# Optimization experiments

Hardware: AMD Instinct MI355X
Metric: run time of the kernel (lower is better)

Reference implementation:

```python
import jax, jax.numpy as jnp
import numpy as np

_DIMS = [("fu1",2,2),("fu2",2,2),("ku1",4,4),("ku2",4,4),("hu1",6,6),("hu2",6,6),("md1",11,16),("md2",16,16),("md3",16,6),("hd1",6,4),("hd2",4,4),("kd1",4,2),("kd2",2,2),("ha1",8,4),("ha2",4,1),("ka1",6,4),("ka2",4,1),("fa1",4,4),("fa2",4,1)]


def setup_inputs() -> dict:
    key = jax.random.key(0)
    B = 2_000_000
    inp = {"x": jax.random.normal(key, (B, 11), dtype=jnp.float32)}
    for i, (name, din, dout) in enumerate(_DIMS):
        kw = jax.random.fold_in(key, i + 1)
        scale = float(np.sqrt(6.0 / (din + dout)))  # xavier_uniform gain=1
        inp[name + "_w"] = jax.random.uniform(kw, (din, dout), jnp.float32, -scale, scale)
        inp[name + "_b"] = jnp.zeros((dout,), jnp.float32)  # nn.Linear default bias ~ small; zeros for determinism
    return inp


def _lin(x, w, b):
    # weights stored as (in, out) == torch W.T
    return x @ w + b


def reference(x, fu1_w, fu1_b, fu2_w, fu2_b, ku1_w, ku1_b, ku2_w, ku2_b, hu1_w, hu1_b, hu2_w, hu2_b, md1_w, md1_b, md2_w, md2_b, md3_w, md3_b, hd1_w, hd1_b, hd2_w, hd2_b, kd1_w, kd1_b, kd2_w, kd2_b, ha1_w, ha1_b, ha2_w, ha2_b, ka1_w, ka1_b, ka2_w, ka2_b, fa1_w, fa1_b, fa2_w, fa2_b):
    r = jax.nn.relu
    h = x[:, 2:3]; k = x[:, 3:4]; f = x[:, 4:5]
    hd = x[:, 8:9]; kd = x[:, 9:10]; fd = x[:, 10:11]
    m_obs = x[:, jnp.array([0, 1, 5, 6, 7])]  # [B,5]
    f_up = r(_lin(r(_lin(jnp.concatenate([f, fd], 1), fu1_w, fu1_b)), fu2_w, fu2_b))            # [B,2]
    k_up = r(_lin(r(_lin(jnp.concatenate([k, kd, f_up], 1), ku1_w, ku1_b)), ku2_w, ku2_b))      # [B,4]
    h_up = r(_lin(r(_lin(jnp.concatenate([h, hd, k_up], 1), hu1_w, hu1_b)), hu2_w, hu2_b))      # [B,6]
    m_in = jnp.concatenate([m_obs, h_up], 1)                                                    # [B,11]
    m_down = r(_lin(r(_lin(r(_lin(m_in, md1_w, md1_b)), md2_w, md2_b)), md3_w, md3_b))          # [B,6]
    h_down = r(_lin(r(_lin(m_down, hd1_w, hd1_b)), hd2_w, hd2_b))                               # [B,4]
    k_down = r(_lin(r(_lin(h_down, kd1_w, kd1_b)), kd2_w, kd2_b))                               # [B,2]
    h_act = _lin(r(_lin(jnp.concatenate([h, hd, m_down], 1), ha1_w, ha1_b)), ha2_w, ha2_b)      # [B,1]
    k_act = _lin(r(_lin(jnp.concatenate([k, kd, h_down], 1), ka1_w, ka1_b)), ka2_w, ka2_b)      # [B,1]
    f_act = _lin(r(_lin(jnp.concatenate([f, fd, k_down], 1), fa1_w, fa1_b)), fa2_w, fa2_b)      # [B,1]
    return jnp.concatenate([h_act, f_act, k_act], 1)                                            # [B,3]
```

## Files before the change

### kernel.cpp

```cpp
#include <hip/hip_runtime.h>

#define BLOCK 256

typedef float v2f __attribute__((ext_vector_type(2)));
typedef unsigned long long u64;

struct WPtrs {
    const float* w[19];
    const float* b[19];
};

enum LId {FU1,FU2,KU1,KU2,HU1,HU2,MD1,MD2,MD3,HD1,HD2,KD1,KD2,HA1,HA2,KA1,KA2,FA1,FA2};

__device__ __forceinline__ void fmaL(v2f& acc, const v2f s, const u64 w) {
    asm("v_pk_fma_f32 %0, %1, %2, %0 op_sel:[0,0,0] op_sel_hi:[0,1,1]"
        : "+v"(acc) : "v"(s), "s"(w));
}
__device__ __forceinline__ void fmaH(v2f& acc, const v2f s, const u64 w) {
    asm("v_pk_fma_f32 %0, %1, %2, %0 op_sel:[1,0,0] op_sel_hi:[1,1,1]"
        : "+v"(acc) : "v"(s), "s"(w));
}
__device__ __forceinline__ v2f pkmax0(const v2f a) {
    const v2f z = {0.0f, 0.0f};
    return __builtin_elementwise_max(a, z);
}
__device__ __forceinline__ v2f bias2(const float* b, int jp) {
    return *reinterpret_cast<const v2f*>(b + 2*jp);
}

__global__ __launch_bounds__(BLOCK) void pnet_kernel(
    const float* __restrict__ x, float* __restrict__ out, int B, WPtrs P) {
    const long long row = (long long)blockIdx.x * BLOCK + threadIdx.x;
    if (row >= B) return;

    const float* pr = x + row * 11;
    const v2f xp01 = *reinterpret_cast<const v2f*>(pr + 0);
    const v2f xp23 = *reinterpret_cast<const v2f*>(pr + 2);
    const v2f xp45 = *reinterpret_cast<const v2f*>(pr + 4);
    const v2f xp67 = *reinterpret_cast<const v2f*>(pr + 6);
    const v2f xp89 = *reinterpret_cast<const v2f*>(pr + 8);
    const v2f xp9A = *reinterpret_cast<const v2f*>(pr + 9);

    v2f fu1p;
    {
        const u64* wp = reinterpret_cast<const u64*>(P.w[FU1]);
        v2f a = bias2(P.b[FU1], 0);
        fmaL(a, xp45, wp[0]);
        fmaH(a, xp9A, wp[1]);
        fu1p = pkmax0(a);
    }
    v2f fup;
    {
        const u64* wp = reinterpret_cast<const u64*>(P.w[FU2]);
        v2f a = bias2(P.b[FU2], 0);
        fmaL(a, fu1p, wp[0]);
        fmaH(a, fu1p, wp[1]);
        fup = pkmax0(a);
    }

    v2f ku1p[2];
    {
        const u64* wp = reinterpret_cast<const u64*>(P.w[KU1]);
#pragma unroll
        for (int jp = 0; jp < 2; ++jp) {
            v2f a = bias2(P.b[KU1], jp);
            fmaH(a, xp23, wp[0*2+jp]);
            fmaH(a, xp89, wp[1*2+jp]);
            fmaL(a, fup,  wp[2*2+jp]);
            fmaH(a, fup,  wp[3*2+jp]);
            ku1p[jp] = pkmax0(a);
        }
    }
    v2f kup[2];
    {
        const u64* wp = reinterpret_cast<const u64*>(P.w[KU2]);
#pragma unroll
        for (int jp = 0; jp < 2; ++jp) {
            v2f a = bias2(P.b[KU2], jp);
            fmaL(a, ku1p[0], wp[0*2+jp]);
            fmaH(a, ku1p[0], wp[1*2+jp]);
            fmaL(a, ku1p[1], wp[2*2+jp]);
            fmaH(a, ku1p[1], wp[3*2+jp]);
            kup[jp] = pkmax0(a);
        }
    }

    v2f hu1p[3];
    {
        const u64* wp = reinterpret_cast<const u64*>(P.w[HU1]);
#pragma unroll
        for (int jp = 0; jp < 3; ++jp) {
            v2f a = bias2(P.b[HU1], jp);
            fmaL(a, xp23,   wp[0*3+jp]);
            fmaL(a, xp89,   wp[1*3+jp]);
            fmaL(a, kup[0], wp[2*3+jp]);
            fmaH(a, kup[0], wp[3*3+jp]);
            fmaL(a, kup[1], wp[4*3+jp]);
            fmaH(a, kup[1], wp[5*3+jp]);
            hu1p[jp] = pkmax0(a);
        }
    }
    v2f hup[3];
    {
        const u64* wp = reinterpret_cast<const u64*>(P.w[HU2]);
#pragma unroll
        for (int jp = 0; jp < 3; ++jp) {
            v2f a = bias2(P.b[HU2], jp);
            fmaL(a, hu1p[0], wp[0*3+jp]);
            fmaH(a, hu1p[0], wp[1*3+jp]);
            fmaL(a, hu1p[1], wp[2*3+jp]);
            fmaH(a, hu1p[1], wp[3*3+jp]);
            fmaL(a, hu1p[2], wp[4*3+jp]);
            fmaH(a, hu1p[2], wp[5*3+jp]);
            hup[jp] = pkmax0(a);
        }
    }

    v2f m1[8];
    {
        const u64* wp = reinterpret_cast<const u64*>(P.w[MD1]);
#pragma unroll
        for (int jp = 0; jp < 8; ++jp) {
            v2f a = bias2(P.b[MD1], jp);
            fmaL(a, xp01,   wp[0*8+jp]);
            fmaH(a, xp01,   wp[1*8+jp]);
            fmaH(a, xp45,   wp[2*8+jp]);
            fmaL(a, xp67,   wp[3*8+jp]);
            fmaH(a, xp67,   wp[4*8+jp]);
            fmaL(a, hup[0], wp[5*8+jp]);
            fmaH(a, hup[0], wp[6*8+jp]);
            fmaL(a, hup[1], wp[7*8+jp]);
            fmaH(a, hup[1], wp[8*8+jp]);
            fmaL(a, hup[2], wp[9*8+jp]);
            fmaH(a, hup[2], wp[10*8+jp]);
            m1[jp] = pkmax0(a);
        }
    }
    v2f m2[8];
    {
        const u64* wp = reinterpret_cast<const u64*>(P.w[MD2]);
#pragma unroll
        for (int jp = 0; jp < 8; ++jp) {
            v2f a = bias2(P.b[MD2], jp);
#pragma unroll
            for (int p = 0; p < 8; ++p) {
                fmaL(a, m1[p], wp[(2*p)  *8+jp]);
                fmaH(a, m1[p], wp[(2*p+1)*8+jp]);
            }
            m2[jp] = pkmax0(a);
        }
    }
    v2f m3[3];
    {
        const u64* wp = reinterpret_cast<const u64*>(P.w[MD3]);
#pragma unroll
        for (int jp = 0; jp < 3; ++jp) {
            v2f a = bias2(P.b[MD3], jp);
#pragma unroll
            for (int p = 0; p < 8; ++p) {
                fmaL(a, m2[p], wp[(2*p)  *3+jp]);
                fmaH(a, m2[p], wp[(2*p+1)*3+jp]);
            }
            m3[jp] = pkmax0(a);
        }
    }

    v2f d1[2];
    {
        const u64* wp = reinterpret_cast<const u64*>(P.w[HD1]);
#pragma unroll
        for (int jp = 0; jp < 2; ++jp) {
            v2f a = bias2(P.b[HD1], jp);
            fmaL(a, m3[0], wp[0*2+jp]);
            fmaH(a, m3[0], wp[1*2+jp]);
            fmaL(a, m3[1], wp[2*2+jp]);
            fmaH(a, m3[1], wp[3*2+jp]);
            fmaL(a, m3[2], wp[4*2+jp]);
            fmaH(a, m3[2], wp[5*2+jp]);
            d1[jp] = pkmax0(a);
        }
    }
    v2f d2[2];
    {
        const u64* wp = reinterpret_cast<const u64*>(P.w[HD2]);
#pragma unroll
        for (int jp = 0; jp < 2; ++jp) {
            v2f a = bias2(P.b[HD2], jp);
            fmaL(a, d1[0], wp[0*2+jp]);
            fmaH(a, d1[0], wp[1*2+jp]);
            fmaL(a, d1[1], wp[2*2+jp]);
            fmaH(a, d1[1], wp[3*2+jp]);
            d2[jp] = pkmax0(a);
        }
    }

    v2f e1;
    {
        const u64* wp = reinterpret_cast<const u64*>(P.w[KD1]);
        v2f a = bias2(P.b[KD1], 0);
        fmaL(a, d2[0], wp[0]);
        fmaH(a, d2[0], wp[1]);
        fmaL(a, d2[1], wp[2]);
        fmaH(a, d2[1], wp[3]);
        e1 = pkmax0(a);
    }
    v2f e2;
    {
        const u64* wp = reinterpret_cast<const u64*>(P.w[KD2]);
        v2f a = bias2(P.b[KD2], 0);
        fmaL(a, e1, wp[0]);
        fmaH(a, e1, wp[1]);
        e2 = pkmax0(a);
    }

    v2f g[2];
    {
        const u64* wp = reinterpret_cast<const u64*>(P.w[HA1]);
#pragma unroll
        for (int jp = 0; jp < 2; ++jp) {
            v2f a = bias2(P.b[HA1], jp);
            fmaL(a, xp23,  wp[0*2+jp]);
            fmaL(a, xp89,  wp[1*2+jp]);
            fmaL(a, m3[0], wp[2*2+jp]);
            fmaH(a, m3[0], wp[3*2+jp]);
            fmaL(a, m3[1], wp[4*2+jp]);
            fmaH(a, m3[1], wp[5*2+jp]);
            fmaL(a, m3[2], wp[6*2+jp]);
            fmaH(a, m3[2], wp[7*2+jp]);
            g[jp] = pkmax0(a);
        }
    }
    const float* wha = P.w[HA2];
    float h_act = P.b[HA2][0];
    h_act = __builtin_fmaf(g[0].x, wha[0], h_act);
    h_act = __builtin_fmaf(g[0].y, wha[1], h_act);
    h_act = __builtin_fmaf(g[1].x, wha[2], h_act);
    h_act = __builtin_fmaf(g[1].y, wha[3], h_act);

    v2f q[2];
    {
        const u64* wp = reinterpret_cast<const u64*>(P.w[KA1]);
#pragma unroll
        for (int jp = 0; jp < 2; ++jp) {
            v2f a = bias2(P.b[KA1], jp);
            fmaH(a, xp23,  wp[0*2+jp]);
            fmaH(a, xp89,  wp[1*2+jp]);
            fmaL(a, d2[0], wp[2*2+jp]);
            fmaH(a, d2[0], wp[3*2+jp]);
            fmaL(a, d2[1], wp[4*2+jp]);
            fmaH(a, d2[1], wp[5*2+jp]);
            q[jp] = pkmax0(a);
        }
    }
    const float* wka = P.w[KA2];
    float k_act = P.b[KA2][0];
    k_act = __builtin_fmaf(q[0].x, wka[0], k_act);
    k_act = __builtin_fmaf(q[0].y, wka[1], k_act);
    k_act = __builtin_fmaf(q[1].x, wka[2], k_act);
    k_act = __builtin_fmaf(q[1].y, wka[3], k_act);

    v2f r[2];
    {
        const u64* wp = reinterpret_cast<const u64*>(P.w[FA1]);
#pragma unroll
        for (int jp = 0; jp < 2; ++jp) {
            v2f a = bias2(P.b[FA1], jp);
            fmaL(a, xp45, wp[0*2+jp]);
            fmaH(a, xp9A, wp[1*2+jp]);
            fmaL(a, e2,   wp[2*2+jp]);
            fmaH(a, e2,   wp[3*2+jp]);
            r[jp] = pkmax0(a);
        }
    }
    const float* wfa = P.w[FA2];
    float f_act = P.b[FA2][0];
    f_act = __builtin_fmaf(r[0].x, wfa[0], f_act);
    f_act = __builtin_fmaf(r[0].y, wfa[1], f_act);
    f_act = __builtin_fmaf(r[1].x, wfa[2], f_act);
    f_act = __builtin_fmaf(r[1].y, wfa[3], f_act);

    float* po = out + row * 3;
    po[0] = h_act;
    po[1] = f_act;
    po[2] = k_act;
}

extern "C" void kernel_launch(void* const* d_in, const int* in_sizes, int n_in,
                              void* d_out, int out_size, void* d_ws, size_t ws_size,
                              hipStream_t stream) {
    const float* x = (const float*)d_in[0];
    float* out = (float*)d_out;
    const int B = in_sizes[0] / 11;

    WPtrs P;
    for (int i = 0; i < 19; ++i) {
        P.w[i] = (const float*)d_in[1 + 2*i];
        P.b[i] = (const float*)d_in[2 + 2*i];
    }

    const int blocks = (int)(((long long)B + BLOCK - 1) / BLOCK);
    pnet_kernel<<<blocks, BLOCK, 0, stream>>>(x, out, B, P);
}
```

Before: 229.6 us.

## Pack all weights and biases into one contiguous stream via prep kernel

Adds a small prep kernel that repacks the 19 layers' weights and biases into a single contiguous workspace buffer, laid out in the order the main kernel reads them (bias pair followed by the weight pairs for each output pair). The main kernel then takes one pointer and uses compile-time offsets. This is meant to turn many scattered scalar loads from 38 separate pointers into sequential wide scalar loads from a single base, cutting SGPR pressure and load instruction count. In exchange it adds a second kernel launch on every call.

```diff
diff --git a/kernel.cpp b/kernel.cpp
--- a/kernel.cpp
+++ b/kernel.cpp
@@ -10,7 +10,36 @@
     const float* b[19];
 };
 
-enum LId {FU1,FU2,KU1,KU2,HU1,HU2,MD1,MD2,MD3,HD1,HD2,KD1,KD2,HA1,HA2,KA1,KA2,FA1,FA2};
+__constant__ const int kDIN[19]  = {2,2,4,4,6,6,11,16,16,6,4,4,2,8,4,6,4,4,4};
+__constant__ const int kDOUT[19] = {2,2,4,4,6,6,16,16,6,4,4,2,2,4,1,4,1,4,1};
+__constant__ const int kOFF[19]  = {0,3,6,16,26,47,68,164,300,351,365,375,380,383,401,404,418,421,431};
+
+__global__ void prep_kernel(WPtrs P, float* __restrict__ ws) {
+    const int l = blockIdx.x;
+    const int t = threadIdx.x;
+    const int din = kDIN[l], dout = kDOUT[l];
+    const int off = kOFF[l];
+    if (dout == 1) {
+        if (t == 0) {
+            float* d = ws + 2*off;
+            d[0] = P.b[l][0];
+            for (int i = 0; i < 4; ++i) d[1+i] = P.w[l][i];
+            d[5] = 0.0f;
+        }
+        return;
+    }
+    const int pairs  = dout >> 1;
+    const int stride = 1 + din;
+    for (int jp = t; jp < pairs; jp += blockDim.x) {
+        float* d = ws + 2*(off + jp*stride);
+        d[0] = P.b[l][2*jp];
+        d[1] = P.b[l][2*jp + 1];
+        for (int i = 0; i < din; ++i) {
+            d[2 + 2*i] = P.w[l][i*dout + 2*jp];
+            d[3 + 2*i] = P.w[l][i*dout + 2*jp + 1];
+        }
+    }
+}
 
 __device__ __forceinline__ void fmaL(v2f& acc, const v2f s, const u64 w) {
     asm("v_pk_fma_f32 %0, %1, %2, %0 op_sel:[0,0,0] op_sel_hi:[0,1,1]"
@@ -24,14 +53,17 @@
     const v2f z = {0.0f, 0.0f};
     return __builtin_elementwise_max(a, z);
 }
-__device__ __forceinline__ v2f bias2(const float* b, int jp) {
-    return *reinterpret_cast<const v2f*>(b + 2*jp);
+__device__ __forceinline__ v2f bcv(const u64 v) {
+    return __builtin_bit_cast(v2f, v);
 }
 
 __global__ __launch_bounds__(BLOCK) void pnet_kernel(
-    const float* __restrict__ x, float* __restrict__ out, int B, WPtrs P) {
+    const float* __restrict__ x, float* __restrict__ out, int B,
+    const float* __restrict__ wstream) {
     const long long row = (long long)blockIdx.x * BLOCK + threadIdx.x;
     if (row >= B) return;
+
+    const u64* W = reinterpret_cast<const u64*>(wstream);
 
     const float* pr = x + row * 11;
     const v2f xp01 = *reinterpret_cast<const v2f*>(pr + 0);
@@ -43,241 +75,210 @@
 
     v2f fu1p;
     {
-        const u64* wp = reinterpret_cast<const u64*>(P.w[FU1]);
-        v2f a = bias2(P.b[FU1], 0);
-        fmaL(a, xp45, wp[0]);
-        fmaH(a, xp9A, wp[1]);
+        v2f a = bcv(W[0]);
+        fmaL(a, xp45, W[1]);
+        fmaH(a, xp9A, W[2]);
         fu1p = pkmax0(a);
     }
     v2f fup;
     {
-        const u64* wp = reinterpret_cast<const u64*>(P.w[FU2]);
-        v2f a = bias2(P.b[FU2], 0);
-        fmaL(a, fu1p, wp[0]);
-        fmaH(a, fu1p, wp[1]);
+        v2f a = bcv(W[3]);
+        fmaL(a, fu1p, W[4]);
+        fmaH(a, fu1p, W[5]);
         fup = pkmax0(a);
     }
 
     v2f ku1p[2];
-    {
-        const u64* wp = reinterpret_cast<const u64*>(P.w[KU1]);
-#pragma unroll
-        for (int jp = 0; jp < 2; ++jp) {
-            v2f a = bias2(P.b[KU1], jp);
-            fmaH(a, xp23, wp[0*2+jp]);
-            fmaH(a, xp89, wp[1*2+jp]);
-            fmaL(a, fup,  wp[2*2+jp]);
-            fmaH(a, fup,  wp[3*2+jp]);
-            ku1p[jp] = pkmax0(a);
+#pragma unroll
+    for (int jp = 0; jp < 2; ++jp) {
+        const int q = 6 + jp*5;
+        v2f a = bcv(W[q]);
+        fmaH(a, xp23, W[q+1]);
+        fmaH(a, xp89, W[q+2]);
+        fmaL(a, fup,  W[q+3]);
+        fmaH(a, fup,  W[q+4]);
+        ku1p[jp] = pkmax0(a);
+    }
+    v2f kup[2];
+#pragma unroll
+    for (int jp = 0; jp < 2; ++jp) {
+        const int q = 16 + jp*5;
+        v2f a = bcv(W[q]);
+        fmaL(a, ku1p[0], W[q+1]);
+        fmaH(a, ku1p[0], W[q+2]);
+        fmaL(a, ku1p[1], W[q+3]);
+        fmaH(a, ku1p[1], W[q+4]);
+        kup[jp] = pkmax0(a);
+    }
+
+    v2f hu1p[3];
+#pragma unroll
+    for (int jp = 0; jp < 3; ++jp) {
+        const int q = 26 + jp*7;
+        v2f a = bcv(W[q]);
+        fmaL(a, xp23,   W[q+1]);
+        fmaL(a, xp89,   W[q+2]);
+        fmaL(a, kup[0], W[q+3]);
+        fmaH(a, kup[0], W[q+4]);
+        fmaL(a, kup[1], W[q+5]);
+        fmaH(a, kup[1], W[q+6]);
+        hu1p[jp] = pkmax0(a);
+    }
+    v2f hup[3];
+#pragma unroll
+    for (int jp = 0; jp < 3; ++jp) {
+        const int q = 47 + jp*7;
+        v2f a = bcv(W[q]);
+        fmaL(a, hu1p[0], W[q+1]);
+        fmaH(a, hu1p[0], W[q+2]);
+        fmaL(a, hu1p[1], W[q+3]);
+        fmaH(a, hu1p[1], W[q+4]);
+        fmaL(a, hu1p[2], W[q+5]);
+        fmaH(a, hu1p[2], W[q+6]);
+        hup[jp] = pkmax0(a);
+    }
+
+    v2f m1[8];
+#pragma unroll
+    for (int jp = 0; jp < 8; ++jp) {
+        const int q = 68 + jp*12;
+        v2f a = bcv(W[q]);
+        fmaL(a, xp01,   W[q+1]);
+        fmaH(a, xp01,   W[q+2]);
+        fmaH(a, xp45,   W[q+3]);
+        fmaL(a, xp67,   W[q+4]);
+        fmaH(a, xp67,   W[q+5]);
+        fmaL(a, hup[0], W[q+6]);
+        fmaH(a, hup[0], W[q+7]);
+        fmaL(a, hup[1], W[q+8]);
+        fmaH(a, hup[1], W[q+9]);
+        fmaL(a, hup[2], W[q+10]);
+        fmaH(a, hup[2], W[q+11]);
+        m1[jp] = pkmax0(a);
+    }
+    v2f m2[8];
+#pragma unroll
+    for (int jp = 0; jp < 8; ++jp) {
+        const int q = 164 + jp*17;
+        v2f a = bcv(W[q]);
+#pragma unroll
+        for (int p = 0; p < 8; ++p) {
+            fmaL(a, m1[p], W[q + 1 + 2*p]);
+            fmaH(a, m1[p], W[q + 2 + 2*p]);
         }
-    }
-    v2f kup[2];
-    {
-        const u64* wp = reinterpret_cast<const u64*>(P.w[KU2]);
-#pragma unroll
-        for (int jp = 0; jp < 2; ++jp) {
-            v2f a = bias2(P.b[KU2], jp);
-            fmaL(a, ku1p[0], wp[0*2+jp]);
-            fmaH(a, ku1p[0], wp[1*2+jp]);
-            fmaL(a, ku1p[1], wp[2*2+jp]);
-            fmaH(a, ku1p[1], wp[3*2+jp]);
-            kup[jp] = pkmax0(a);
+        m2[jp] = pkmax0(a);
+    }
+    v2f m3[3];
+#pragma unroll
+    for (int jp = 0; jp < 3; ++jp) {
+        const int q = 300 + jp*17;
+        v2f a = bcv(W[q]);
+#pragma unroll
+        for (int p = 0; p < 8; ++p) {
+            fmaL(a, m2[p], W[q + 1 + 2*p]);
+            fmaH(a, m2[p], W[q + 2 + 2*p]);
         }
-    }
-
-    v2f hu1p[3];
-    {
-        const u64* wp = reinterpret_cast<const u64*>(P.w[HU1]);
-#pragma unroll
-        for (int jp = 0; jp < 3; ++jp) {
-            v2f a = bias2(P.b[HU1], jp);
-            fmaL(a, xp23,   wp[0*3+jp]);
-            fmaL(a, xp89,   wp[1*3+jp]);
-            fmaL(a, kup[0], wp[2*3+jp]);
-            fmaH(a, kup[0], wp[3*3+jp]);
-            fmaL(a, kup[1], wp[4*3+jp]);
-            fmaH(a, kup[1], wp[5*3+jp]);
-            hu1p[jp] = pkmax0(a);
-        }
-    }
-    v2f hup[3];
-    {
-        const u64* wp = reinterpret_cast<const u64*>(P.w[HU2]);
-#pragma unroll
-        for (int jp = 0; jp < 3; ++jp) {
-            v2f a = bias2(P.b[HU2], jp);
-            fmaL(a, hu1p[0], wp[0*3+jp]);
-            fmaH(a, hu1p[0], wp[1*3+jp]);
-            fmaL(a, hu1p[1], wp[2*3+jp]);
-            fmaH(a, hu1p[1], wp[3*3+jp]);
-            fmaL(a, hu1p[2], wp[4*3+jp]);
-            fmaH(a, hu1p[2], wp[5*3+jp]);
-            hup[jp] = pkmax0(a);
-        }
-    }
-
-    v2f m1[8];
-    {
-        const u64* wp = reinterpret_cast<const u64*>(P.w[MD1]);
-#pragma unroll
-        for (int jp = 0; jp < 8; ++jp) {
-            v2f a = bias2(P.b[MD1], jp);
-            fmaL(a, xp01,   wp[0*8+jp]);
-            fmaH(a, xp01,   wp[1*8+jp]);
-            fmaH(a, xp45,   wp[2*8+jp]);
-            fmaL(a, xp67,   wp[3*8+jp]);
-            fmaH(a, xp67,   wp[4*8+jp]);
-            fmaL(a, hup[0], wp[5*8+jp]);
-            fmaH(a, hup[0], wp[6*8+jp]);
-            fmaL(a, hup[1], wp[7*8+jp]);
-            fmaH(a, hup[1], wp[8*8+jp]);
-            fmaL(a, hup[2], wp[9*8+jp]);
-            fmaH(a, hup[2], wp[10*8+jp]);
-            m1[jp] = pkmax0(a);
-        }
-    }
-    v2f m2[8];
-    {
-        const u64* wp = reinterpret_cast<const u64*>(P.w[MD2]);
-#pragma unroll
-        for (int jp = 0; jp < 8; ++jp) {
-            v2f a = bias2(P.b[MD2], jp);
-#pragma unroll
-            for (int p = 0; p < 8; ++p) {
-                fmaL(a, m1[p], wp[(2*p)  *8+jp]);
-                fmaH(a, m1[p], wp[(2*p+1)*8+jp]);
-            }
-            m2[jp] = pkmax0(a);
-        }
-    }
-    v2f m3[3];
-    {
-        const u64* wp = reinterpret_cast<const u64*>(P.w[MD3]);
-#pragma unroll
-        for (int jp = 0; jp < 3; ++jp) {
-            v2f a = bias2(P.b[MD3], jp);
-#pragma unroll
-            for (int p = 0; p < 8; ++p) {
-                fmaL(a, m2[p], wp[(2*p)  *3+jp]);
-                fmaH(a, m2[p], wp[(2*p+1)*3+jp]);
-            }
-            m3[jp] = pkmax0(a);
-        }
+        m3[jp] = pkmax0(a);
     }
 
     v2f d1[2];
-    {
-        const u64* wp = reinterpret_cast<const u64*>(P.w[HD1]);
-#pragma unroll
-        for (int jp = 0; jp < 2; ++jp) {
-            v2f a = bias2(P.b[HD1], jp);
-            fmaL(a, m3[0], wp[0*2+jp]);
-            fmaH(a, m3[0], wp[1*2+jp]);
-            fmaL(a, m3[1], wp[2*2+jp]);
-            fmaH(a, m3[1], wp[3*2+jp]);
-            fmaL(a, m3[2], wp[4*2+jp]);
-            fmaH(a, m3[2], wp[5*2+jp]);
-            d1[jp] = pkmax0(a);
-        }
+#pragma unroll
+    for (int jp = 0; jp < 2; ++jp) {
+        const int q = 351 + jp*7;
+        v2f a = bcv(W[q]);
+        fmaL(a, m3[0], W[q+1]);
+        fmaH(a, m3[0], W[q+2]);
+        fmaL(a, m3[1], W[q+3]);
+        fmaH(a, m3[1], W[q+4]);
+        fmaL(a, m3[2], W[q+5]);
+        fmaH(a, m3[2], W[q+6]);
+        d1[jp] = pkmax0(a);
     }
     v2f d2[2];
-    {
-        const u64* wp = reinterpret_cast<const u64*>(P.w[HD2]);
-#pragma unroll
-        for (int jp = 0; jp < 2; ++jp) {
-            v2f a = bias2(P.b[HD2], jp);
-            fmaL(a, d1[0], wp[0*2+jp]);
-            fmaH(a, d1[0], wp[1*2+jp]);
-            fmaL(a, d1[1], wp[2*2+jp]);
-            fmaH(a, d1[1], wp[3*2+jp]);
-            d2[jp] = pkmax0(a);
-        }
+#pragma unroll
+    for (int jp = 0; jp < 2; ++jp) {
+        const int q = 365 + jp*5;
+        v2f a = bcv(W[q]);
+        fmaL(a, d1[0], W[q+1]);
+        fmaH(a, d1[0], W[q+2]);
+        fmaL(a, d1[1], W[q+3]);
+        fmaH(a, d1[1], W[q+4]);
+        d2[jp] = pkmax0(a);
     }
 
     v2f e1;
     {
-        const u64* wp = reinterpret_cast<const u64*>(P.w[KD1]);
-        v2f a = bias2(P.b[KD1], 0);
-        fmaL(a, d2[0], wp[0]);
-        fmaH(a, d2[0], wp[1]);
-        fmaL(a, d2[1], wp[2]);
-        fmaH(a, d2[1], wp[3]);
+        v2f a = bcv(W[375]);
+        fmaL(a, d2[0], W[376]);
+        fmaH(a, d2[0], W[377]);
+        fmaL(a, d2[1], W[378]);
+        fmaH(a, d2[1], W[379]);
         e1 = pkmax0(a);
     }
     v2f e2;
     {
-        const u64* wp = reinterpret_cast<const u64*>(P.w[KD2]);
-        v2f a = bias2(P.b[KD2], 0);
-        fmaL(a, e1, wp[0]);
-        fmaH(a, e1, wp[1]);
+        v2f a = bcv(W[380]);
+        fmaL(a, e1, W[381]);
+        fmaH(a, e1, W[382]);
         e2 = pkmax0(a);
     }
 
     v2f g[2];
-    {
-        const u64* wp = reinterpret_cast<const u64*>(P.w[HA1]);
-#pragma unroll
-        for (int jp = 0; jp < 2; ++jp) {
-            v2f a = bias2(P.b[HA1], jp);
-            fmaL(a, xp23,  wp[0*2+jp]);
-            fmaL(a, xp89,  wp[1*2+jp]);
-            fmaL(a, m3[0], wp[2*2+jp]);
-            fmaH(a, m3[0], wp[3*2+jp]);
-            fmaL(a, m3[1], wp[4*2+jp]);
-            fmaH(a, m3[1], wp[5*2+jp]);
-            fmaL(a, m3[2], wp[6*2+jp]);
-            fmaH(a, m3[2], wp[7*2+jp]);
-            g[jp] = pkmax0(a);
-        }
-    }
-    const float* wha = P.w[HA2];
-    float h_act = P.b[HA2][0];
-    h_act = __builtin_fmaf(g[0].x, wha[0], h_act);
-    h_act = __builtin_fmaf(g[0].y, wha[1], h_act);
-    h_act = __builtin_fmaf(g[1].x, wha[2], h_act);
-    h_act = __builtin_fmaf(g[1].y, wha[3], h_act);
-
-    v2f q[2];
-    {
-        const u64* wp = reinterpret_cast<const u64*>(P.w[KA1]);
-#pragma unroll
-        for (int jp = 0; jp < 2; ++jp) {
-            v2f a = bias2(P.b[KA1], jp);
-            fmaH(a, xp23,  wp[0*2+jp]);
-            fmaH(a, xp89,  wp[1*2+jp]);
-            fmaL(a, d2[0], wp[2*2+jp]);
-            fmaH(a, d2[0], wp[3*2+jp]);
-            fmaL(a, d2[1], wp[4*2+jp]);
-            fmaH(a, d2[1], wp[5*2+jp]);
-            q[jp] = pkmax0(a);
-        }
-    }
-    const float* wka = P.w[KA2];
-    float k_act = P.b[KA2][0];
-    k_act = __builtin_fmaf(q[0].x, wka[0], k_act);
-    k_act = __builtin_fmaf(q[0].y, wka[1], k_act);
-    k_act = __builtin_fmaf(q[1].x, wka[2], k_act);
-    k_act = __builtin_fmaf(q[1].y, wka[3], k_act);
+#pragma unroll
+    for (int jp = 0; jp < 2; ++jp) {
+        const int q = 383 + jp*9;
+        v2f a = bcv(W[q]);
+        fmaL(a, xp23,  W[q+1]);
+        fmaL(a, xp89,  W[q+2]);
+        fmaL(a, m3[0], W[q+3]);
+        fmaH(a, m3[0], W[q+4]);
+        fmaL(a, m3[1], W[q+5]);
+        fmaH(a, m3[1], W[q+6]);
+        fmaL(a, m3[2], W[q+7]);
+        fmaH(a, m3[2], W[q+8]);
+        g[jp] = pkmax0(a);
+    }
+    float h_act = wstream[802];
+    h_act = __builtin_fmaf(g[0].x, wstream[803], h_act);
+    h_act = __builtin_fmaf(g[0].y, wstream[804], h_act);
+    h_act = __builtin_fmaf(g[1].x, wstream[805], h_act);
+    h_act = __builtin_fmaf(g[1].y, wstream[806], h_act);
+
+    v2f q2[2];
+#pragma unroll
+    for (int jp = 0; jp < 2; ++jp) {
+        const int q = 404 + jp*7;
+        v2f a = bcv(W[q]);
+        fmaH(a, xp23,  W[q+1]);
+        fmaH(a, xp89,  W[q+2]);
+        fmaL(a, d2[0], W[q+3]);
+        fmaH(a, d2[0], W[q+4]);
+        fmaL(a, d2[1], W[q+5]);
+        fmaH(a, d2[1], W[q+6]);
+        q2[jp] = pkmax0(a);
+    }
+    float k_act = wstream[836];
+    k_act = __builtin_fmaf(q2[0].x, wstream[837], k_act);
+    k_act = __builtin_fmaf(q2[0].y, wstream[838], k_act);
+    k_act = __builtin_fmaf(q2[1].x, wstream[839], k_act);
+    k_act = __builtin_fmaf(q2[1].y, wstream[840], k_act);
 
     v2f r[2];
-    {
-        const u64* wp = reinterpret_cast<const u64*>(P.w[FA1]);
-#pragma unroll
-        for (int jp = 0; jp < 2; ++jp) {
-            v2f a = bias2(P.b[FA1], jp);
-            fmaL(a, xp45, wp[0*2+jp]);
-            fmaH(a, xp9A, wp[1*2+jp]);
-            fmaL(a, e2,   wp[2*2+jp]);
-            fmaH(a, e2,   wp[3*2+jp]);
-            r[jp] = pkmax0(a);
-        }
-    }
-    const float* wfa = P.w[FA2];
-    float f_act = P.b[FA2][0];
-    f_act = __builtin_fmaf(r[0].x, wfa[0], f_act);
-    f_act = __builtin_fmaf(r[0].y, wfa[1], f_act);
-    f_act = __builtin_fmaf(r[1].x, wfa[2], f_act);
-    f_act = __builtin_fmaf(r[1].y, wfa[3], f_act);
+#pragma unroll
+    for (int jp = 0; jp < 2; ++jp) {
+        const int q = 421 + jp*5;
+        v2f a = bcv(W[q]);
+        fmaL(a, xp45, W[q+1]);
+        fmaH(a, xp9A, W[q+2]);
+        fmaL(a, e2,   W[q+3]);
+        fmaH(a, e2,   W[q+4]);
+        r[jp] = pkmax0(a);
+    }
+    float f_act = wstream[862];
+    f_act = __builtin_fmaf(r[0].x, wstream[863], f_act);
+    f_act = __builtin_fmaf(r[0].y, wstream[864], f_act);
+    f_act = __builtin_fmaf(r[1].x, wstream[865], f_act);
+    f_act = __builtin_fmaf(r[1].y, wstream[866], f_act);
 
     float* po = out + row * 3;
     po[0] = h_act;
@@ -298,6 +299,9 @@
         P.b[i] = (const float*)d_in[2 + 2*i];
     }
 
+    float* ws = (float*)d_ws;
+    prep_kernel<<<19, 32, 0, stream>>>(P, ws);
+
     const int blocks = (int)(((long long)B + BLOCK - 1) / BLOCK);
-    pnet_kernel<<<blocks, BLOCK, 0, stream>>>(x, out, B, P);
-}
+    pnet_kernel<<<blocks, BLOCK, 0, stream>>>(x, out, B, ws);
+}
```

After: 224.6 us. -2.2%, faster.
